# Optimization experiments

Measured on AMD Instinct MI355X. Metric: run time of the kernel, lower is better.

The kernel has to match this reference:

```python
import jax, jax.numpy as jnp
import numpy as np

LEAK = 0.2  # negative_slope of F.leaky_relu in the torch module
AVG_DEG = 32.0


def _linear_params(key, out_d, in_d):
    # torch nn.Linear default init: U(-1/sqrt(in), 1/sqrt(in))
    s = 1.0 / np.sqrt(in_d)
    k1, k2 = jax.random.split(key)
    W = jax.random.uniform(k1, (out_d, in_d), jnp.float32, -s, s)
    b = jax.random.uniform(k2, (out_d,), jnp.float32, -s, s)
    return W, b


def setup_inputs() -> dict:
    key = jax.random.key(0)
    ks = jax.random.split(key, 8)
    N, D_in, D_h, D_out = 8192, 128, 128, 64
    x = jax.random.normal(ks[0], (N, D_in), jnp.float32)
    # random sparse graph, avg out-degree ~32, stored densely as the module does
    adj = (jax.random.uniform(ks[1], (N, N), jnp.float32) < (AVG_DEG / N)).astype(jnp.float32)
    W0, b0 = _linear_params(ks[2], D_h, D_in)
    aW0, ab0 = _linear_params(ks[3], 1, 2 * D_h)
    W1, b1 = _linear_params(ks[4], D_h, D_h)
    aW1, ab1 = _linear_params(ks[5], 1, 2 * D_h)
    W2, b2 = _linear_params(ks[6], D_out, D_h)
    aW2, ab2 = _linear_params(ks[7], 1, 2 * D_out)
    return dict(x=x, adj=adj,
                W0=W0, b0=b0, aW0=aW0, ab0=ab0,
                W1=W1, b1=b1, aW1=aW1, ab1=ab1,
                W2=W2, b2=b2, aW2=aW2, ab2=ab2)


def _attn_layer(x, adj, W, b, aW, ab):
    # h = leaky_relu(Linear(x)), [N, F]
    h = jax.nn.leaky_relu(x @ W.T + b, LEAK)
    N = x.shape[0]
    F = h.shape[1]
    # e[i,j] = attn(concat(h[i], h[j])) -- avoid materializing [N,N,2F]
    el = h @ aW[0, :F]   # [N]
    er = h @ aW[0, F:]   # [N]
    e = el[:, None] + er[None, :] + ab[0]  # [N, N]
    # denominator trick from the source: sum_j exp(e*A) counts 1 per non-neighbor,
    # then -N + out_degree removes those, leaving sum over neighbors of exp(e).
    deg = jnp.sum(adj, axis=1)  # out_degrees
    denom = jnp.sum(jnp.exp(e * adj), axis=1) - jnp.float32(N) + deg  # [N]
    alpha = jnp.exp(e) / denom[:, None] * adj  # masked softmax over neighbors
    h2 = alpha @ h  # [N, F] aggregation
    return jax.nn.relu(h2)  # self.activation


def reference(x, adj, W0, b0, aW0, ab0, W1, b1, aW1, ab1, W2, b2, aW2, ab2):
    h = _attn_layer(x, adj, W0, b0, aW0, ab0)
    h = _attn_layer(h, adj, W1, b1, aW1, ab1)
    h = _attn_layer(h, adj, W2, b2, aW2, ab2)
    return h
```

## Files before the change

kernel.cpp:

```cpp
#include <hip/hip_runtime.h>

#define LEAK 0.2f
#define NROW 8192
#define KDIM 128
#define MAXD 128
#define TPB  1024
#define NBLK 512

#define OF_FLAG 0x0ul
#define OF_CNT  0x1000ul
#define OF_EL1  0x10000ul
#define OF_ER1  0x18000ul
#define OF_EL2  0x20000ul
#define OF_ER2  0x28000ul
#define OF_EL3  0x30000ul
#define OF_ER3  0x38000ul
#define OF_HB1  0x100000ul
#define OF_HB2  0x300000ul
#define OF_HB3  0x500000ul
#define OF_NBR  0x700000ul

typedef __attribute__((ext_vector_type(8))) short bf16x8;
typedef __attribute__((ext_vector_type(4))) float f32x4;

__device__ __forceinline__ float b2f(unsigned short u) {
  return __uint_as_float(((unsigned)u) << 16);
}
__device__ __forceinline__ unsigned short f2b(float f) {
  unsigned u = __float_as_uint(f);
  return (unsigned short)((u + 0x7FFFu + ((u >> 16) & 1u)) >> 16);
}
__device__ __forceinline__ float ld_any(const void* p, long i, int isb) {
  return isb ? b2f(((const unsigned short*)p)[i]) : ((const float*)p)[i];
}

__device__ __forceinline__ int detect_isb(const void* adj, int* sflag) {
  const uint4* a4 = (const uint4*)adj;
  if (threadIdx.x == 0) *sflag = 0;
  __syncthreads();
  unsigned any = 0;
  #pragma unroll
  for (int i = 0; i < 4; ++i) {
    uint4 v = a4[threadIdx.x + i * TPB];
    any |= (v.x | v.y | v.z | v.w);
  }
  if (any & 0xFFFFu) atomicOr(sflag, 1);
  __syncthreads();
  return *sflag;
}

__device__ __forceinline__ bf16x8 ldA(const void* X, long off, int isb) {
  if (isb) return *(const bf16x8*)((const unsigned short*)X + off);
  const float* f = (const float*)X + off;
  float4 p0 = *(const float4*)f;
  float4 p1 = *(const float4*)(f + 4);
  bf16x8 o;
  ((unsigned short*)&o)[0] = f2b(p0.x); ((unsigned short*)&o)[1] = f2b(p0.y);
  ((unsigned short*)&o)[2] = f2b(p0.z); ((unsigned short*)&o)[3] = f2b(p0.w);
  ((unsigned short*)&o)[4] = f2b(p1.x); ((unsigned short*)&o)[5] = f2b(p1.y);
  ((unsigned short*)&o)[6] = f2b(p1.z); ((unsigned short*)&o)[7] = f2b(p1.w);
  return o;
}

__device__ __forceinline__ void emit_f32(uint4 v, int cb, int& cnt, unsigned short* nb,
                                         unsigned long long ltm) {
  unsigned u[4] = {v.x, v.y, v.z, v.w};
  #pragma unroll
  for (int q = 0; q < 4; ++q) {
    int nz = u[q] != 0;
    unsigned long long m = __ballot(nz);
    if (nz) { int p = cnt + __popcll(m & ltm); if (p < MAXD) nb[p] = (unsigned short)(cb + q); }
    cnt += __popcll(m);
  }
}
__device__ __forceinline__ void emit_b16(uint4 v, int cb, int& cnt, unsigned short* nb,
                                         unsigned long long ltm) {
  unsigned u[4] = {v.x, v.y, v.z, v.w};
  #pragma unroll
  for (int q = 0; q < 4; ++q)
    #pragma unroll
    for (int k = 0; k < 2; ++k) {
      int nz = ((u[q] >> (16 * k)) & 0xFFFFu) != 0;
      unsigned long long m = __ballot(nz);
      if (nz) { int p = cnt + __popcll(m & ltm); if (p < MAXD) nb[p] = (unsigned short)(cb + q * 2 + k); }
      cnt += __popcll(m);
    }
}

__device__ __forceinline__ void nbrs_body(const void* adj, unsigned short* nbr, int* cnts,
                                          int isb, int row, int lane) {
  unsigned long long ltm = (1ull << lane) - 1ull;
  unsigned short* nb = nbr + (long)row * MAXD;
  int cnt = 0;
  if (isb) {
    const uint4* base = (const uint4*)((const char*)adj + (long)row * (NROW * 2));
    #pragma unroll 1
    for (int t = 0; t < 16; t += 4) {
      uint4 v0 = base[(t + 0) * 64 + lane];
      uint4 v1 = base[(t + 1) * 64 + lane];
      uint4 v2 = base[(t + 2) * 64 + lane];
      uint4 v3 = base[(t + 3) * 64 + lane];
      emit_b16(v0, (t + 0) * 512 + lane * 8, cnt, nb, ltm);
      emit_b16(v1, (t + 1) * 512 + lane * 8, cnt, nb, ltm);
      emit_b16(v2, (t + 2) * 512 + lane * 8, cnt, nb, ltm);
      emit_b16(v3, (t + 3) * 512 + lane * 8, cnt, nb, ltm);
    }
  } else {
    const uint4* base = (const uint4*)((const char*)adj + (long)row * (NROW * 4));
    #pragma unroll 1
    for (int t = 0; t < 32; t += 4) {
      uint4 v0 = base[(t + 0) * 64 + lane];
      uint4 v1 = base[(t + 1) * 64 + lane];
      uint4 v2 = base[(t + 2) * 64 + lane];
      uint4 v3 = base[(t + 3) * 64 + lane];
      emit_f32(v0, (t + 0) * 256 + lane * 4, cnt, nb, ltm);
      emit_f32(v1, (t + 1) * 256 + lane * 4, cnt, nb, ltm);
      emit_f32(v2, (t + 2) * 256 + lane * 4, cnt, nb, ltm);
      emit_f32(v3, (t + 3) * 256 + lane * 4, cnt, nb, ltm);
    }
  }
  if (lane == 0) cnts[row] = (cnt < MAXD ? cnt : MAXD);
}

template<int FIN>
__device__ __forceinline__ float2 agg_row(const void* HBv, const float* ER, float eli,
                                          const unsigned short* nb, int cnt, int lane) {
  const unsigned* HBU = (const unsigned*)HBv;
  const unsigned short* HBS = (const unsigned short*)HBv;
  float acc0 = 0.f, acc1 = 0.f, den = 0.f;
  for (int t0 = 0; t0 < cnt; t0 += 64) {
    int nrem = min(64, cnt - t0);
    int j = 0; float wv = 0.f;
    if (lane < nrem) { j = nb[t0 + lane]; wv = expf(eli + ER[j]); }
    int t = 0;
    for (; t + 4 <= nrem; t += 4) {
      float w0 = __shfl(wv, t),     w1 = __shfl(wv, t + 1);
      float w2 = __shfl(wv, t + 2), w3 = __shfl(wv, t + 3);
      int j0 = __shfl(j, t),     j1 = __shfl(j, t + 1);
      int j2 = __shfl(j, t + 2), j3 = __shfl(j, t + 3);
      den += (w0 + w1) + (w2 + w3);
      if (FIN == 128) {
        unsigned h0 = HBU[(long)j0 * 64 + lane], h1 = HBU[(long)j1 * 64 + lane];
        unsigned h2 = HBU[(long)j2 * 64 + lane], h3 = HBU[(long)j3 * 64 + lane];
        acc0 += w0 * b2f((unsigned short)h0) + w1 * b2f((unsigned short)h1)
              + w2 * b2f((unsigned short)h2) + w3 * b2f((unsigned short)h3);
        acc1 += w0 * b2f((unsigned short)(h0 >> 16)) + w1 * b2f((unsigned short)(h1 >> 16))
              + w2 * b2f((unsigned short)(h2 >> 16)) + w3 * b2f((unsigned short)(h3 >> 16));
      } else {
        float h0 = b2f(HBS[(long)j0 * 64 + lane]), h1 = b2f(HBS[(long)j1 * 64 + lane]);
        float h2 = b2f(HBS[(long)j2 * 64 + lane]), h3 = b2f(HBS[(long)j3 * 64 + lane]);
        acc0 += w0 * h0 + w1 * h1 + w2 * h2 + w3 * h3;
      }
    }
    for (; t < nrem; ++t) {
      float wt = __shfl(wv, t);
      int jt = __shfl(j, t);
      den += wt;
      if (FIN == 128) {
        unsigned hv = HBU[(long)jt * 64 + lane];
        acc0 += wt * b2f((unsigned short)hv);
        acc1 += wt * b2f((unsigned short)(hv >> 16));
      } else {
        acc0 += wt * b2f(HBS[(long)jt * 64 + lane]);
      }
    }
  }
  float inv = (den > 0.f) ? 1.f / den : 0.f;
  float v0 = acc0 * inv; v0 = v0 > 0.f ? v0 : 0.f;
  float v1 = acc1 * inv; v1 = v1 > 0.f ? v1 : 0.f;
  return make_float2(v0, v1);
}

template<int NCT, int AMODE>
__device__ __forceinline__ void gemm_compute(const void* Xg, const unsigned* aT,
    const void* W, const void* bia, const void* aW, unsigned short* HBo,
    float (*sEL)[16], float (*sER)[16], int isb, int row0, int w, int lane) {
  if (w >= NCT) return;
  constexpr int FOUT = NCT * 16;
  int r = lane & 15;
  int k0 = (lane >> 4) * 8;
  f32x4 acc = {0.f, 0.f, 0.f, 0.f};
  #pragma unroll
  for (int kb = 0; kb < KDIM; kb += 32) {
    bf16x8 a;
    if (AMODE == 1) {
      a = ldA(Xg, (long)(row0 + r) * KDIM + k0 + kb, isb);
    } else {
      int cb = ((k0 + kb) >> 1) ^ ((r & 7) << 2);
      a = *(const bf16x8*)(aT + r * 64 + cb);
    }
    bf16x8 bfr = ldA(W, (long)(w * 16 + r) * KDIM + k0 + kb, isb);
    acc = __builtin_amdgcn_mfma_f32_16x16x32_bf16(a, bfr, acc, 0, 0, 0);
  }
  int colg = w * 16 + r;
  float bb = ld_any(bia, colg, isb);
  float al = ld_any(aW, colg, isb);
  float ar = ld_any(aW, FOUT + colg, isb);
  #pragma unroll
  for (int j = 0; j < 4; ++j) {
    int rloc = (lane >> 4) * 4 + j;
    float v = acc[j] + bb;
    v = v > 0.f ? v : LEAK * v;
    HBo[(long)(row0 + rloc) * FOUT + colg] = f2b(v);
    float tl = v * al, tr = v * ar;
    #pragma unroll
    for (int m = 1; m < 16; m <<= 1) { tl += __shfl_xor(tl, m); tr += __shfl_xor(tr, m); }
    if (r == 0) { sEL[w][rloc] = tl; sER[w][rloc] = tr; }
  }
}

template<int NCT>
__device__ __forceinline__ void elr_reduce(float* ELo, float* ERo,
    float (*sEL)[16], float (*sER)[16], int row0) {
  if (threadIdx.x < 16) {
    float sl = 0.f, sr = 0.f;
    #pragma unroll
    for (int q = 0; q < NCT; ++q) { sl += sEL[q][threadIdx.x]; sr += sER[q][threadIdx.x]; }
    ELo[row0 + threadIdx.x] = sl;
    ERo[row0 + threadIdx.x] = sr;
  }
}

__global__ __launch_bounds__(TPB, 8) void k1(const void* __restrict__ adj,
    const void* __restrict__ x, const void* __restrict__ W0,
    const void* __restrict__ b0, const void* __restrict__ aW0, char* __restrict__ ws) {
  __shared__ float sEL[8][16], sER[8][16];
  __shared__ int sflag;
  int isb = detect_isb(adj, &sflag);
  if (threadIdx.x == 0) *(int*)(ws + OF_FLAG) = isb;
  int w = threadIdx.x >> 6, lane = threadIdx.x & 63, row0 = blockIdx.x * 16;
  nbrs_body(adj, (unsigned short*)(ws + OF_NBR), (int*)(ws + OF_CNT), isb, row0 + w, lane);
  gemm_compute<8, 1>(x, nullptr, W0, b0, aW0,
                     (unsigned short*)(ws + OF_HB1), sEL, sER, isb, row0, w, lane);
  __syncthreads();
  elr_reduce<8>((float*)(ws + OF_EL1), (float*)(ws + OF_ER1), sEL, sER, row0);
}

__global__ __launch_bounds__(TPB, 8) void k2(const void* __restrict__ W1,
    const void* __restrict__ b1, const void* __restrict__ aW1,
    const void* __restrict__ ab0, char* __restrict__ ws) {
  __shared__ unsigned aTile[16 * 64];
  __shared__ float sEL[8][16], sER[8][16];
  int isb = *(const int*)(ws + OF_FLAG);
  int w = threadIdx.x >> 6, lane = threadIdx.x & 63, row0 = blockIdx.x * 16;
  int row = row0 + w;
  float abv = ld_any(ab0, 0, isb);
  float2 v = agg_row<128>(ws + OF_HB1, (const float*)(ws + OF_ER1),
                          ((const float*)(ws + OF_EL1))[row] + abv,
                          (const unsigned short*)(ws + OF_NBR) + (long)row * MAXD,
                          ((const int*)(ws + OF_CNT))[row], lane);
  aTile[w * 64 + (lane ^ ((w & 7) << 2))] = ((unsigned)f2b(v.y) << 16) | (unsigned)f2b(v.x);
  __syncthreads();
  gemm_compute<8, 0>(nullptr, aTile, W1, b1, aW1,
                     (unsigned short*)(ws + OF_HB2), sEL, sER, isb, row0, w, lane);
  __syncthreads();
  elr_reduce<8>((float*)(ws + OF_EL2), (float*)(ws + OF_ER2), sEL, sER, row0);
}

__global__ __launch_bounds__(TPB, 8) void k3(const void* __restrict__ W2,
    const void* __restrict__ b2, const void* __restrict__ aW2,
    const void* __restrict__ ab1, char* __restrict__ ws) {
  __shared__ unsigned aTile[16 * 64];
  __shared__ float sEL[8][16], sER[8][16];
  int isb = *(const int*)(ws + OF_FLAG);
  int w = threadIdx.x >> 6, lane = threadIdx.x & 63, row0 = blockIdx.x * 16;
  int row = row0 + w;
  float abv = ld_any(ab1, 0, isb);
  float2 v = agg_row<128>(ws + OF_HB2, (const float*)(ws + OF_ER2),
                          ((const float*)(ws + OF_EL2))[row] + abv,
                          (const unsigned short*)(ws + OF_NBR) + (long)row * MAXD,
                          ((const int*)(ws + OF_CNT))[row], lane);
  aTile[w * 64 + (lane ^ ((w & 7) << 2))] = ((unsigned)f2b(v.y) << 16) | (unsigned)f2b(v.x);
  __syncthreads();
  gemm_compute<4, 0>(nullptr, aTile, W2, b2, aW2,
                     (unsigned short*)(ws + OF_HB3), sEL, sER, isb, row0, w, lane);
  __syncthreads();
  elr_reduce<4>((float*)(ws + OF_EL3), (float*)(ws + OF_ER3), sEL, sER, row0);
}

__global__ __launch_bounds__(TPB, 8) void k4(const void* __restrict__ ab2,
    char* __restrict__ ws, void* __restrict__ out) {
  int isb = *(const int*)(ws + OF_FLAG);
  int w = threadIdx.x >> 6, lane = threadIdx.x & 63;
  int row = blockIdx.x * 16 + w;
  float abv = ld_any(ab2, 0, isb);
  float2 v = agg_row<64>(ws + OF_HB3, (const float*)(ws + OF_ER3),
                         ((const float*)(ws + OF_EL3))[row] + abv,
                         (const unsigned short*)(ws + OF_NBR) + (long)row * MAXD,
                         ((const int*)(ws + OF_CNT))[row], lane);
  if (isb) ((unsigned short*)out)[(long)row * 64 + lane] = f2b(v.x);
  else     ((float*)out)[(long)row * 64 + lane] = v.x;
}

extern "C" void kernel_launch(void* const* d_in, const int* in_sizes, int n_in,
                              void* d_out, int out_size, void* d_ws, size_t ws_size,
                              hipStream_t stream) {
  char* ws = (char*)d_ws;
  const void* x   = d_in[0];
  const void* adj = d_in[1];
  const void* W0 = d_in[2];  const void* b0 = d_in[3];  const void* aW0 = d_in[4];  const void* ab0 = d_in[5];
  const void* W1 = d_in[6];  const void* b1 = d_in[7];  const void* aW1 = d_in[8];  const void* ab1 = d_in[9];
  const void* W2 = d_in[10]; const void* b2 = d_in[11]; const void* aW2 = d_in[12]; const void* ab2 = d_in[13];

  k1<<<NBLK, TPB, 0, stream>>>(adj, x, W0, b0, aW0, ws);
  k2<<<NBLK, TPB, 0, stream>>>(W1, b1, aW1, ab0, ws);
  k3<<<NBLK, TPB, 0, stream>>>(W2, b2, aW2, ab1, ws);
  k4<<<NBLK, TPB, 0, stream>>>(ab2, ws, d_out);
}
```

Before: 94.22 us.

## Fuse layers two and three plus final aggregation into one cooperative kernel

Replaces the three trailing kernel launches with a single cooperative launch that runs the three phases back to back, separated by software grid barriers built on agent-scope atomics in the workspace. Barrier counters are zeroed by the first kernel. The aim is to remove kernel launch gaps and tail drain between dependent phases. In exchange it adds atomic spin-waits and host-side device attribute queries on every call. It falls back to the separate launches if cooperative launch is unavailable or fails.

Measured after the change: 259.5 us. +175.4%, slower.

```diff
diff --git a/kernel.cpp b/kernel.cpp
--- a/kernel.cpp
+++ b/kernel.cpp
@@ -15,6 +15,7 @@
 #define OF_ER2  0x28000ul
 #define OF_EL3  0x30000ul
 #define OF_ER3  0x38000ul
+#define OF_BAR  0x40000ul
 #define OF_HB1  0x100000ul
 #define OF_HB2  0x300000ul
 #define OF_HB3  0x500000ul
@@ -47,6 +48,22 @@
   if (any & 0xFFFFu) atomicOr(sflag, 1);
   __syncthreads();
   return *sflag;
+}
+
+__device__ __forceinline__ void grid_barrier(int* cnt, int* rel) {
+  __syncthreads();
+  if (threadIdx.x == 0) {
+    __threadfence();
+    int old = __hip_atomic_fetch_add(cnt, 1, __ATOMIC_ACQ_REL, __HIP_MEMORY_SCOPE_AGENT);
+    if (old == NBLK - 1) {
+      __hip_atomic_store(rel, 1, __ATOMIC_RELEASE, __HIP_MEMORY_SCOPE_AGENT);
+    } else {
+      while (__hip_atomic_load(rel, __ATOMIC_ACQUIRE, __HIP_MEMORY_SCOPE_AGENT) == 0)
+        __builtin_amdgcn_s_sleep(8);
+    }
+    __threadfence();
+  }
+  __syncthreads();
 }
 
 __device__ __forceinline__ bf16x8 ldA(const void* X, long off, int isb) {
@@ -221,28 +238,9 @@
   }
 }
 
-__global__ __launch_bounds__(TPB, 8) void k1(const void* __restrict__ adj,
-    const void* __restrict__ x, const void* __restrict__ W0,
-    const void* __restrict__ b0, const void* __restrict__ aW0, char* __restrict__ ws) {
-  __shared__ float sEL[8][16], sER[8][16];
-  __shared__ int sflag;
-  int isb = detect_isb(adj, &sflag);
-  if (threadIdx.x == 0) *(int*)(ws + OF_FLAG) = isb;
-  int w = threadIdx.x >> 6, lane = threadIdx.x & 63, row0 = blockIdx.x * 16;
-  nbrs_body(adj, (unsigned short*)(ws + OF_NBR), (int*)(ws + OF_CNT), isb, row0 + w, lane);
-  gemm_compute<8, 1>(x, nullptr, W0, b0, aW0,
-                     (unsigned short*)(ws + OF_HB1), sEL, sER, isb, row0, w, lane);
-  __syncthreads();
-  elr_reduce<8>((float*)(ws + OF_EL1), (float*)(ws + OF_ER1), sEL, sER, row0);
-}
-
-__global__ __launch_bounds__(TPB, 8) void k2(const void* __restrict__ W1,
-    const void* __restrict__ b1, const void* __restrict__ aW1,
-    const void* __restrict__ ab0, char* __restrict__ ws) {
-  __shared__ unsigned aTile[16 * 64];
-  __shared__ float sEL[8][16], sER[8][16];
-  int isb = *(const int*)(ws + OF_FLAG);
-  int w = threadIdx.x >> 6, lane = threadIdx.x & 63, row0 = blockIdx.x * 16;
+__device__ __forceinline__ void phaseA(const void* W1, const void* b1, const void* aW1,
+    const void* ab0, char* ws, unsigned* aTile, float (*sEL)[16], float (*sER)[16],
+    int isb, int w, int lane, int row0) {
   int row = row0 + w;
   float abv = ld_any(ab0, 0, isb);
   float2 v = agg_row<128>(ws + OF_HB1, (const float*)(ws + OF_ER1),
@@ -256,14 +254,9 @@
   __syncthreads();
   elr_reduce<8>((float*)(ws + OF_EL2), (float*)(ws + OF_ER2), sEL, sER, row0);
 }
-
-__global__ __launch_bounds__(TPB, 8) void k3(const void* __restrict__ W2,
-    const void* __restrict__ b2, const void* __restrict__ aW2,
-    const void* __restrict__ ab1, char* __restrict__ ws) {
-  __shared__ unsigned aTile[16 * 64];
-  __shared__ float sEL[8][16], sER[8][16];
-  int isb = *(const int*)(ws + OF_FLAG);
-  int w = threadIdx.x >> 6, lane = threadIdx.x & 63, row0 = blockIdx.x * 16;
+__device__ __forceinline__ void phaseB(const void* W2, const void* b2, const void* aW2,
+    const void* ab1, char* ws, unsigned* aTile, float (*sEL)[16], float (*sER)[16],
+    int isb, int w, int lane, int row0) {
   int row = row0 + w;
   float abv = ld_any(ab1, 0, isb);
   float2 v = agg_row<128>(ws + OF_HB2, (const float*)(ws + OF_ER2),
@@ -277,12 +270,9 @@
   __syncthreads();
   elr_reduce<4>((float*)(ws + OF_EL3), (float*)(ws + OF_ER3), sEL, sER, row0);
 }
-
-__global__ __launch_bounds__(TPB, 8) void k4(const void* __restrict__ ab2,
-    char* __restrict__ ws, void* __restrict__ out) {
-  int isb = *(const int*)(ws + OF_FLAG);
-  int w = threadIdx.x >> 6, lane = threadIdx.x & 63;
-  int row = blockIdx.x * 16 + w;
+__device__ __forceinline__ void phaseC(const void* ab2, char* ws, void* out,
+    int isb, int w, int lane, int row0) {
+  int row = row0 + w;
   float abv = ld_any(ab2, 0, isb);
   float2 v = agg_row<64>(ws + OF_HB3, (const float*)(ws + OF_ER3),
                          ((const float*)(ws + OF_EL3))[row] + abv,
@@ -290,6 +280,66 @@
                          ((const int*)(ws + OF_CNT))[row], lane);
   if (isb) ((unsigned short*)out)[(long)row * 64 + lane] = f2b(v.x);
   else     ((float*)out)[(long)row * 64 + lane] = v.x;
+}
+
+__global__ __launch_bounds__(TPB, 8) void k1(const void* __restrict__ adj,
+    const void* __restrict__ x, const void* __restrict__ W0,
+    const void* __restrict__ b0, const void* __restrict__ aW0, char* __restrict__ ws) {
+  __shared__ float sEL[8][16], sER[8][16];
+  __shared__ int sflag;
+  int isb = detect_isb(adj, &sflag);
+  if (threadIdx.x == 0) {
+    *(int*)(ws + OF_FLAG) = isb;
+    if (blockIdx.x == 0) {
+      int* bar = (int*)(ws + OF_BAR);
+      bar[0] = bar[1] = bar[2] = bar[3] = 0;
+    }
+  }
+  int w = threadIdx.x >> 6, lane = threadIdx.x & 63, row0 = blockIdx.x * 16;
+  nbrs_body(adj, (unsigned short*)(ws + OF_NBR), (int*)(ws + OF_CNT), isb, row0 + w, lane);
+  gemm_compute<8, 1>(x, nullptr, W0, b0, aW0,
+                     (unsigned short*)(ws + OF_HB1), sEL, sER, isb, row0, w, lane);
+  __syncthreads();
+  elr_reduce<8>((float*)(ws + OF_EL1), (float*)(ws + OF_ER1), sEL, sER, row0);
+}
+
+__global__ __launch_bounds__(TPB, 8) void kf(const void* W1, const void* b1,
+    const void* aW1, const void* ab0, const void* W2, const void* b2,
+    const void* aW2, const void* ab1, const void* ab2, char* ws, void* out) {
+  __shared__ unsigned aTile[16 * 64];
+  __shared__ float sEL[8][16], sER[8][16];
+  int isb = *(const int*)(ws + OF_FLAG);
+  int w = threadIdx.x >> 6, lane = threadIdx.x & 63, row0 = blockIdx.x * 16;
+  int* bar = (int*)(ws + OF_BAR);
+  phaseA(W1, b1, aW1, ab0, ws, aTile, sEL, sER, isb, w, lane, row0);
+  grid_barrier(bar + 0, bar + 1);
+  phaseB(W2, b2, aW2, ab1, ws, aTile, sEL, sER, isb, w, lane, row0);
+  grid_barrier(bar + 2, bar + 3);
+  phaseC(ab2, ws, out, isb, w, lane, row0);
+}
+
+__global__ __launch_bounds__(TPB, 8) void k2(const void* __restrict__ W1,
+    const void* __restrict__ b1, const void* __restrict__ aW1,
+    const void* __restrict__ ab0, char* __restrict__ ws) {
+  __shared__ unsigned aTile[16 * 64];
+  __shared__ float sEL[8][16], sER[8][16];
+  int isb = *(const int*)(ws + OF_FLAG);
+  phaseA(W1, b1, aW1, ab0, ws, aTile, sEL, sER, isb,
+         threadIdx.x >> 6, threadIdx.x & 63, blockIdx.x * 16);
+}
+__global__ __launch_bounds__(TPB, 8) void k3(const void* __restrict__ W2,
+    const void* __restrict__ b2, const void* __restrict__ aW2,
+    const void* __restrict__ ab1, char* __restrict__ ws) {
+  __shared__ unsigned aTile[16 * 64];
+  __shared__ float sEL[8][16], sER[8][16];
+  int isb = *(const int*)(ws + OF_FLAG);
+  phaseB(W2, b2, aW2, ab1, ws, aTile, sEL, sER, isb,
+         threadIdx.x >> 6, threadIdx.x & 63, blockIdx.x * 16);
+}
+__global__ __launch_bounds__(TPB, 8) void k4(const void* __restrict__ ab2,
+    char* __restrict__ ws, void* __restrict__ out) {
+  int isb = *(const int*)(ws + OF_FLAG);
+  phaseC(ab2, ws, out, isb, threadIdx.x >> 6, threadIdx.x & 63, blockIdx.x * 16);
 }
 
 extern "C" void kernel_launch(void* const* d_in, const int* in_sizes, int n_in,
@@ -301,9 +351,26 @@
   const void* W0 = d_in[2];  const void* b0 = d_in[3];  const void* aW0 = d_in[4];  const void* ab0 = d_in[5];
   const void* W1 = d_in[6];  const void* b1 = d_in[7];  const void* aW1 = d_in[8];  const void* ab1 = d_in[9];
   const void* W2 = d_in[10]; const void* b2 = d_in[11]; const void* aW2 = d_in[12]; const void* ab2 = d_in[13];
+  void* outp = d_out;
 
   k1<<<NBLK, TPB, 0, stream>>>(adj, x, W0, b0, aW0, ws);
-  k2<<<NBLK, TPB, 0, stream>>>(W1, b1, aW1, ab0, ws);
-  k3<<<NBLK, TPB, 0, stream>>>(W2, b2, aW2, ab1, ws);
-  k4<<<NBLK, TPB, 0, stream>>>(ab2, ws, d_out);
-}
+
+  int dev = 0, coop = 0;
+  (void)hipGetDevice(&dev);
+  (void)hipDeviceGetAttribute(&coop, hipDeviceAttributeCooperativeLaunch, dev);
+  bool ok = false;
+  if (coop) {
+    void* args[11] = {(void*)&W1, (void*)&b1, (void*)&aW1, (void*)&ab0,
+                      (void*)&W2, (void*)&b2, (void*)&aW2, (void*)&ab1,
+                      (void*)&ab2, (void*)&ws, (void*)&outp};
+    hipError_t e = hipLaunchCooperativeKernel((void*)kf, dim3(NBLK), dim3(TPB),
+                                              args, 0, stream);
+    ok = (e == hipSuccess);
+    if (!ok) (void)hipGetLastError();
+  }
+  if (!ok) {
+    k2<<<NBLK, TPB, 0, stream>>>(W1, b1, aW1, ab0, ws);
+    k3<<<NBLK, TPB, 0, stream>>>(W2, b2, aW2, ab1, ws);
+    k4<<<NBLK, TPB, 0, stream>>>(ab2, ws, outp);
+  }
+}
```
